# Optimization experiments

Measured on AMD Instinct MI355X. Metric: run time of the kernel, lower is better.

Reference implementation:

```python
import jax, jax.numpy as jnp
import numpy as np

K_MSG = 1024   # message length k (rows of G)
N_CODE = 2048  # codeword length n (cols of G)
B = 32768      # number of message blocks


def setup_inputs() -> dict:
    key = jax.random.key(0)
    kb, kg = jax.random.split(key)
    b = jax.random.randint(kb, (B, K_MSG), 0, 2, dtype=jnp.int32)
    G = jax.random.randint(kg, (K_MSG, N_CODE), 0, 2, dtype=jnp.int32)
    return {"b": b, "G": G}


def reference(b, G):
    # GF(2) linear block encode: c = (b @ G) mod 2
    # b: [num_blocks, k] bits (0/1), G: [k, n] generator matrix (0/1)
    b2 = b.astype(jnp.int32)
    G2 = G.astype(jnp.int32)
    c = jnp.mod(jnp.matmul(b2, G2), 2)  # [num_blocks, n]
    return c.astype(jnp.int32)
```

## Files before the change

### kernel.cpp

```cpp
#include <hip/hip_runtime.h>
#include <stdint.h>

typedef unsigned long long u64;
typedef unsigned int u32;
typedef u32 v4u __attribute__((ext_vector_type(4)));

#define K_MSG   1024
#define N_CODE  2048
#define NB      32768
#define KW      16
#define ROWS_TILE 256
#define COLS_PER_BLOCK 256

__global__ void pack_b_kernel(const int* __restrict__ b, u64* __restrict__ bp,
                              int nwords) {
    const int lane  = threadIdx.x & 63;
    const int wave  = blockIdx.x * (blockDim.x >> 6) + (threadIdx.x >> 6);
    const int nwave = gridDim.x * (blockDim.x >> 6);
    for (int word = wave; word < nwords; word += nwave) {
        int v = b[(size_t)word * 64 + lane];
        u64 m = __ballot((v & 1) != 0);
        if (lane == 0) bp[word] = m;
    }
}

__global__ void pack_g_kernel(const int* __restrict__ G, u64* __restrict__ gp) {
    const int lane = threadIdx.x & 63;
    const int wave = blockIdx.x * (blockDim.x >> 6) + (threadIdx.x >> 6);
    const int w    = wave >> 5;
    const int jb   = wave & 31;
    const int j    = jb * 64 + lane;
    u64 word = 0;
#pragma unroll 16
    for (int t = 0; t < 64; ++t) {
        int v = G[(size_t)(w * 64 + t) * N_CODE + j];
        word |= (u64)(v & 1) << t;
    }
    gp[(size_t)w * N_CODE + j] = word;
}

__global__ __launch_bounds__(256, 4) void encode_main(const u64* __restrict__ bp,
                                                      const u64* __restrict__ gp,
                                                      int* __restrict__ out) {
    __shared__ u32 rows[ROWS_TILE * 32];

    const int tid = threadIdx.x;
    const int j   = blockIdx.x * COLS_PER_BLOCK + tid;
    const int r0  = blockIdx.y * ROWS_TILE;

    u32 g[32];
#pragma unroll
    for (int w = 0; w < KW; ++w) {
        u64 v = gp[(size_t)w * N_CODE + j];
        g[2 * w]     = (u32)v;
        g[2 * w + 1] = (u32)(v >> 32);
    }

    {
        const v4u* __restrict__ src = (const v4u*)(bp + ((size_t)r0 << 4));
        v4u* dst = (v4u*)rows;
#pragma unroll
        for (int i = 0; i < 8; ++i)
            dst[tid + COLS_PER_BLOCK * i] = src[tid + COLS_PER_BLOCK * i];
    }
    __syncthreads();

    int* __restrict__ op = out + (size_t)r0 * N_CODE + j;

#pragma unroll 2
    for (int r = 0; r < ROWS_TILE; ++r) {
        const u32* rw = &rows[r * 32];
        u32 a0 = 0, a1 = 0, a2 = 0, a3 = 0;
#pragma unroll
        for (int i = 0; i < 8; ++i) {
            a0 ^= rw[i]      & g[i];
            a1 ^= rw[8 + i]  & g[8 + i];
            a2 ^= rw[16 + i] & g[16 + i];
            a3 ^= rw[24 + i] & g[24 + i];
        }
        u32 acc = (a0 ^ a1) ^ (a2 ^ a3);
        op[(size_t)r * N_CODE] = (int)(__popc(acc) & 1);
    }
}

__global__ void encode_naive(const int* __restrict__ b, const int* __restrict__ G,
                             int* __restrict__ out) {
    size_t idx = (size_t)blockIdx.x * blockDim.x + threadIdx.x;
    size_t total = (size_t)NB * N_CODE;
    if (idx >= total) return;
    int i = (int)(idx / N_CODE);
    int j = (int)(idx % N_CODE);
    int acc = 0;
    for (int k = 0; k < K_MSG; ++k)
        acc ^= b[(size_t)i * K_MSG + k] & G[(size_t)k * N_CODE + j];
    out[idx] = acc & 1;
}

extern "C" void kernel_launch(void* const* d_in, const int* in_sizes, int n_in,
                              void* d_out, int out_size, void* d_ws, size_t ws_size,
                              hipStream_t stream) {
    const int* b = (const int*)d_in[0];
    const int* G = (const int*)d_in[1];
    int* out = (int*)d_out;

    const size_t bp_bytes = (size_t)NB * KW * sizeof(u64);
    const size_t gp_bytes = (size_t)N_CODE * KW * sizeof(u64);

    if (ws_size < bp_bytes + gp_bytes) {
        size_t total = (size_t)NB * N_CODE;
        encode_naive<<<(unsigned)((total + 255) / 256), 256, 0, stream>>>(b, G, out);
        return;
    }

    u64* bp = (u64*)d_ws;
    u64* gp = (u64*)((char*)d_ws + bp_bytes);

    pack_b_kernel<<<2048, 256, 0, stream>>>(b, bp, NB * KW);
    pack_g_kernel<<<128, 256, 0, stream>>>(G, gp);

    dim3 grid(N_CODE / COLS_PER_BLOCK, NB / ROWS_TILE);
    encode_main<<<grid, 256, 0, stream>>>(bp, gp, out);
}
```

Baseline: 159.5 us.

## Compute four output columns per thread with vectorized stores and int4 b packing

Each thread now holds generator bits for four columns (128 registers) and reuses every LDS row word across them, writing results as 128-bit stores. The b packing loads int4 per lane, which permutes the bit order inside each word, and the G packing is reordered to match. This cuts LDS reads per output and store instruction count, but register pressure rises, so occupancy drops to 2 blocks per SIMD and the grid shrinks to 2x256 blocks.

```diff
diff --git a/kernel.cpp b/kernel.cpp
--- a/kernel.cpp
+++ b/kernel.cpp
@@ -4,23 +4,31 @@
 typedef unsigned long long u64;
 typedef unsigned int u32;
 typedef u32 v4u __attribute__((ext_vector_type(4)));
+typedef int v4i __attribute__((ext_vector_type(4)));
 
 #define K_MSG   1024
 #define N_CODE  2048
 #define NB      32768
 #define KW      16
-#define ROWS_TILE 256
-#define COLS_PER_BLOCK 256
+#define ROWS_TILE 128
+#define COLS_TILE 1024
 
-__global__ void pack_b_kernel(const int* __restrict__ b, u64* __restrict__ bp,
-                              int nwords) {
+
+__global__ void pack_b_kernel(const int* __restrict__ b, u64* __restrict__ bp) {
     const int lane  = threadIdx.x & 63;
     const int wave  = blockIdx.x * (blockDim.x >> 6) + (threadIdx.x >> 6);
     const int nwave = gridDim.x * (blockDim.x >> 6);
-    for (int word = wave; word < nwords; word += nwave) {
-        int v = b[(size_t)word * 64 + lane];
-        u64 m = __ballot((v & 1) != 0);
-        if (lane == 0) bp[word] = m;
+    const int niter = NB * 4;
+    for (int idx = wave; idx < niter; idx += nwave) {
+        int4 v = *(const int4*)(b + (size_t)idx * 256 + lane * 4);
+        u64 m0 = __ballot((v.x & 1) != 0);
+        u64 m1 = __ballot((v.y & 1) != 0);
+        u64 m2 = __ballot((v.z & 1) != 0);
+        u64 m3 = __ballot((v.w & 1) != 0);
+        if (lane == 0) {
+            u64* d = bp + (size_t)idx * 4;
+            d[0] = m0; d[1] = m1; d[2] = m2; d[3] = m3;
+        }
     }
 }
 
@@ -30,56 +38,66 @@
     const int w    = wave >> 5;
     const int jb   = wave & 31;
     const int j    = jb * 64 + lane;
+    const int g    = w >> 2;
+    const int s    = w & 3;
     u64 word = 0;
 #pragma unroll 16
     for (int t = 0; t < 64; ++t) {
-        int v = G[(size_t)(w * 64 + t) * N_CODE + j];
+        int v = G[(size_t)(g * 256 + 4 * t + s) * N_CODE + j];
         word |= (u64)(v & 1) << t;
     }
     gp[(size_t)w * N_CODE + j] = word;
 }
 
-__global__ __launch_bounds__(256, 4) void encode_main(const u64* __restrict__ bp,
+__global__ __launch_bounds__(256, 2) void encode_main(const u64* __restrict__ bp,
                                                       const u64* __restrict__ gp,
                                                       int* __restrict__ out) {
-    __shared__ u32 rows[ROWS_TILE * 32];
+    __shared__ v4u rows_v[ROWS_TILE * 8];
+    u32* rows = (u32*)rows_v;
 
     const int tid = threadIdx.x;
-    const int j   = blockIdx.x * COLS_PER_BLOCK + tid;
+    const int j0  = blockIdx.x * COLS_TILE + tid * 4;
     const int r0  = blockIdx.y * ROWS_TILE;
 
-    u32 g[32];
+    u32 g[4][32];
 #pragma unroll
     for (int w = 0; w < KW; ++w) {
-        u64 v = gp[(size_t)w * N_CODE + j];
-        g[2 * w]     = (u32)v;
-        g[2 * w + 1] = (u32)(v >> 32);
+        v4u q0 = *(const v4u*)(gp + (size_t)w * N_CODE + j0);
+        v4u q1 = *(const v4u*)(gp + (size_t)w * N_CODE + j0 + 2);
+        g[0][2 * w] = q0.x; g[0][2 * w + 1] = q0.y;
+        g[1][2 * w] = q0.z; g[1][2 * w + 1] = q0.w;
+        g[2][2 * w] = q1.x; g[2][2 * w + 1] = q1.y;
+        g[3][2 * w] = q1.z; g[3][2 * w + 1] = q1.w;
     }
 
     {
         const v4u* __restrict__ src = (const v4u*)(bp + ((size_t)r0 << 4));
-        v4u* dst = (v4u*)rows;
 #pragma unroll
-        for (int i = 0; i < 8; ++i)
-            dst[tid + COLS_PER_BLOCK * i] = src[tid + COLS_PER_BLOCK * i];
+        for (int i = 0; i < 4; ++i)
+            rows_v[tid + 256 * i] = src[tid + 256 * i];
     }
     __syncthreads();
 
-    int* __restrict__ op = out + (size_t)r0 * N_CODE + j;
+    int* __restrict__ op = out + (size_t)r0 * N_CODE + j0;
 
 #pragma unroll 2
     for (int r = 0; r < ROWS_TILE; ++r) {
         const u32* rw = &rows[r * 32];
-        u32 a0 = 0, a1 = 0, a2 = 0, a3 = 0;
+        v4i res;
 #pragma unroll
-        for (int i = 0; i < 8; ++i) {
-            a0 ^= rw[i]      & g[i];
-            a1 ^= rw[8 + i]  & g[8 + i];
-            a2 ^= rw[16 + i] & g[16 + i];
-            a3 ^= rw[24 + i] & g[24 + i];
+        for (int c = 0; c < 4; ++c) {
+            u32 x0 = 0, x1 = 0, x2 = 0, x3 = 0;
+#pragma unroll
+            for (int i = 0; i < 8; ++i) {
+                x0 ^= rw[i]      & g[c][i];
+                x1 ^= rw[8 + i]  & g[c][8 + i];
+                x2 ^= rw[16 + i] & g[c][16 + i];
+                x3 ^= rw[24 + i] & g[c][24 + i];
+            }
+            u32 acc = (x0 ^ x1) ^ (x2 ^ x3);
+            res[c] = (int)(__popc(acc) & 1);
         }
-        u32 acc = (a0 ^ a1) ^ (a2 ^ a3);
-        op[(size_t)r * N_CODE] = (int)(__popc(acc) & 1);
+        *(v4i*)(op + (size_t)r * N_CODE) = res;
     }
 }
 
@@ -115,9 +133,9 @@
     u64* bp = (u64*)d_ws;
     u64* gp = (u64*)((char*)d_ws + bp_bytes);
 
-    pack_b_kernel<<<2048, 256, 0, stream>>>(b, bp, NB * KW);
+    pack_b_kernel<<<2048, 256, 0, stream>>>(b, bp);
     pack_g_kernel<<<128, 256, 0, stream>>>(G, gp);
 
-    dim3 grid(N_CODE / COLS_PER_BLOCK, NB / ROWS_TILE);
+    dim3 grid(N_CODE / COLS_TILE, NB / ROWS_TILE);
     encode_main<<<grid, 256, 0, stream>>>(bp, gp, out);
 }
```

New measurement: 160.9 us. No clear change (+0.9%).
